# Kernel tuning notes

Hardware: AMD Instinct MI355X
Metric: run time of the kernel (lower is better)

Reference implementation:

```python
import jax, jax.numpy as jnp
import numpy as np

N_NODES = 50000
IN_DIM = 256
HID = 128
OUT_DIM = 64
N_LAYERS = 3
N_EDGES = 800000
BATCH = 4096
BN_EPS = 1e-5
LRELU_SLOPE = 0.01


def setup_inputs() -> dict:
    key = jax.random.key(0)
    ks = jax.random.split(key, 24)
    inp = {}
    inp["x"] = jax.random.normal(ks[0], (N_NODES, IN_DIM), jnp.float32)
    inp["edge_index"] = jax.random.randint(ks[1], (2, N_EDGES), 0, N_NODES, dtype=jnp.int32)
    inp["drug_pos_ids"] = jax.random.randint(ks[2], (BATCH,), 0, N_NODES, dtype=jnp.int32)
    inp["target_pos_ids"] = jax.random.randint(ks[3], (BATCH,), 0, N_NODES, dtype=jnp.int32)
    inp["drug_neg_ids"] = jax.random.randint(ks[4], (BATCH,), 0, N_NODES, dtype=jnp.int32)
    inp["target_neg_ids"] = jax.random.randint(ks[5], (BATCH,), 0, N_NODES, dtype=jnp.int32)
    inp["adjacency_matrix"] = jnp.zeros((1, 1), jnp.float32)  # dead arg in original forward
    # GCN layer params (xavier-normal-ish scale, zero bias as in __init__)
    for i in range(N_LAYERS):
        din = IN_DIM if i == 0 else HID
        inp[f"gcn_w{i}"] = jax.random.normal(ks[6 + i], (HID, din), jnp.float32) * np.float32(np.sqrt(2.0 / (din + HID)))
        inp[f"gcn_b{i}"] = jnp.zeros((HID,), jnp.float32)
    inp["bn_gamma"] = jnp.ones((HID,), jnp.float32)
    inp["bn_beta"] = jnp.zeros((HID,), jnp.float32)
    inp["W_D"] = jax.random.normal(ks[10], (HID, HID), jnp.float32) * np.float32(np.sqrt(2.0 / HID))
    inp["W_T"] = jax.random.normal(ks[11], (HID, HID), jnp.float32) * np.float32(np.sqrt(2.0 / HID))
    inp["q_D"] = jax.random.normal(ks[12], (HID,), jnp.float32)
    inp["q_T"] = jax.random.normal(ks[13], (HID,), jnp.float32)
    inp["out_w"] = jax.random.normal(ks[14], (OUT_DIM, HID), jnp.float32) * np.float32(np.sqrt(1.0 / HID))
    inp["out_b"] = jnp.zeros((OUT_DIM,), jnp.float32)
    return inp


def gcn_conv(x, w, b, src, dst, num_nodes):
    # PyG GCNConv: h = x @ W^T, then symmetric-normalized aggregation with self-loops
    h = x @ w.T                                           # [N, HID]
    deg = 1.0 + jax.ops.segment_sum(jnp.ones(src.shape[0], h.dtype), dst, num_segments=num_nodes)
    dinv = jax.lax.rsqrt(deg)                             # [N]
    norm = dinv[src] * dinv[dst]                          # [E]
    agg = jax.ops.segment_sum(h[src] * norm[:, None], dst, num_segments=num_nodes)
    agg = agg + h * (dinv * dinv)[:, None]                # self-loop contribution
    return agg + b


def batchnorm(x, gamma, beta):
    # training-mode BatchNorm1d math (batch statistics, biased var)
    mean = jnp.mean(x, axis=0)
    var = jnp.mean(jnp.square(x - mean), axis=0)
    return (x - mean) * jax.lax.rsqrt(var + BN_EPS) * gamma + beta


def attention_pooling(emb, W, q):
    # emb: [L, N, H]; softmax over the layer axis L
    h = jax.nn.leaky_relu(jnp.einsum('lnh,kh->lnk', emb, W), negative_slope=LRELU_SLOPE)
    e = jnp.einsum('lnk,k->ln', h, q)                     # [L, N]
    alpha = jax.nn.softmax(e, axis=0)
    return jnp.einsum('lnh,ln->nh', emb, alpha)           # [N, H]


def reference(x, edge_index, drug_pos_ids, target_pos_ids, drug_neg_ids, target_neg_ids,
              adjacency_matrix, gcn_w0, gcn_b0, gcn_w1, gcn_b1, gcn_w2, gcn_b2,
              bn_gamma, bn_beta, W_D, W_T, q_D, q_T, out_w, out_b):
    src, dst = edge_index[0], edge_index[1]
    num_nodes = x.shape[0]
    gcn_params = [(gcn_w0, gcn_b0), (gcn_w1, gcn_b1), (gcn_w2, gcn_b2)]
    layer_embs = []
    h = x
    for w, b in gcn_params:
        h = jax.nn.relu(gcn_conv(h, w, b, src, dst, num_nodes))
        h = batchnorm(h, bn_gamma, bn_beta)
        # dropout: identity (eval mode)
        layer_embs.append(h)
    emb = jnp.stack(layer_embs, axis=0)                   # [L, N, H]
    z_D = attention_pooling(emb, W_D, q_D) @ out_w.T + out_b
    z_T = attention_pooling(emb, W_T, q_T) @ out_w.T + out_b
    return (z_D[drug_pos_ids], z_T[target_pos_ids], z_D[drug_neg_ids], z_T[target_neg_ids])
```

## Files before the change

kernel.cpp:

```cpp
#include <hip/hip_runtime.h>
#include <hip/hip_fp16.h>
#include <cstdint>

#define N_NODES 50000
#define IN_DIM  256
#define HID     128
#define OUT_DIM 64
#define N_EDGES 800000
#define BATCH   4096
#define BN_EPS  1e-5f
#define SLOPE   0.01f

typedef unsigned short u16;
typedef __attribute__((ext_vector_type(8))) short bf16x8;
typedef __attribute__((ext_vector_type(4))) float f32x4;

__device__ __forceinline__ u16 f2bf(float f) {
    union { float f; unsigned u; } v; v.f = f;
    unsigned r = v.u + 0x7FFF + ((v.u >> 16) & 1);
    return (u16)(r >> 16);
}
__device__ __forceinline__ float bf2f(u16 b) {
    union { unsigned u; float f; } v; v.u = ((unsigned)b) << 16;
    return v.f;
}
__device__ __forceinline__ void splitbf(float v, u16* hi, u16* lo) {
    u16 h = f2bf(v);
    *hi = h;
    *lo = f2bf(v - bf2f(h));
}

__device__ __forceinline__ void swz_store(u16* __restrict__ buf, int K, int n, int k, float v) {
    int KC = K >> 7;
    int chunk = (n >> 6) * KC + (k >> 7);
    int base = chunk * 16384 + ((n >> 4) & 3) * 2048 + ((k >> 5) & 3) * 512
             + (((k >> 3) & 3) * 16 + (n & 15)) * 8 + (k & 7);
    u16 hi, lo;
    splitbf(v, &hi, &lo);
    buf[base] = hi;
    buf[base + 8192] = lo;
}

#define BNP_SPREAD 64
#define BNACC_PER_LAYER (BNP_SPREAD * 256)


#define PW0 (HID * IN_DIM)
#define PW1 (PW0 + HID * HID)
#define PW2 (PW1 + HID * HID)
#define PWD (PW2 + HID * HID)
#define PWT (PWD + HID * HID)
#define POW (PWT + OUT_DIM * HID)
#define PBN (POW + 3 * BNACC_PER_LAYER)
#define PBC (PBN + 256)
#define PTOT (PBC + 2 * 3 * 2 * BATCH)

__global__ void prep(const float* __restrict__ w0, const float* __restrict__ w1,
                     const float* __restrict__ w2, const float* __restrict__ WD,
                     const float* __restrict__ WT, const float* __restrict__ out_w,
                     u16* __restrict__ w0swz, u16* __restrict__ w1swz, u16* __restrict__ w2swz,
                     u16* __restrict__ wDTswz,
                     float* __restrict__ wt, float* __restrict__ bnacc3,
                     int* __restrict__ bucketCnt, float* __restrict__ ebuf) {
    int i = blockIdx.x * 256 + threadIdx.x;
    if (i < PW0) {
        swz_store(w0swz, IN_DIM, i >> 8, i & 255, w0[i]);
    } else if (i < PW1) {
        int j = i - PW0; swz_store(w1swz, HID, j >> 7, j & 127, w1[j]);
    } else if (i < PW2) {
        int j = i - PW1; swz_store(w2swz, HID, j >> 7, j & 127, w2[j]);
    } else if (i < PWD) {
        int j = i - PW2; swz_store(wDTswz, HID, j >> 7, j & 127, WD[j]);
    } else if (i < PWT) {
        int j = i - PWD; swz_store(wDTswz + 32768, HID, j >> 7, j & 127, WT[j]);
    } else if (i < POW) {
        int j = i - PWT;
        wt[j] = out_w[(j & 63) * HID + (j >> 6)];
    } else if (i < PBN) {
        bnacc3[i - POW] = 0.f;
    } else if (i < PBC) {
        bucketCnt[i - PBN] = 0;
    } else if (i < PTOT) {
        ebuf[i - PBC] = 0.f;
    }
}


#define NBKT 196
#define PASSA_CHUNK 2048
#define NB_A ((N_EDGES + PASSA_CHUNK - 1) / PASSA_CHUNK)

__global__ void bucket_count(const int* __restrict__ dst, int* __restrict__ bucketCnt) {
    __shared__ int hist[NBKT];
    int t = threadIdx.x;
    if (t < NBKT) hist[t] = 0;
    __syncthreads();
    int b0 = blockIdx.x * PASSA_CHUNK;
    int b1 = min(b0 + PASSA_CHUNK, N_EDGES);
    for (int i = b0 + t; i < b1; i += 256)
        atomicAdd(&hist[dst[i] >> 8], 1);
    __syncthreads();
    if (t < NBKT && hist[t] > 0) atomicAdd(&bucketCnt[t], hist[t]);
}

__global__ void bucket_scan(const int* __restrict__ bucketCnt, int* __restrict__ bucketBase,
                            int* __restrict__ gcursor, int* __restrict__ rowstart) {
    __shared__ int s[256];
    int t = threadIdx.x;
    int v = (t < NBKT) ? bucketCnt[t] : 0;
    s[t] = v;
    __syncthreads();
#pragma unroll
    for (int off = 1; off < 256; off <<= 1) {
        int tmp = (t >= off) ? s[t - off] : 0;
        __syncthreads();
        s[t] += tmp;
        __syncthreads();
    }
    if (t < NBKT) { bucketBase[t] = s[t] - v; gcursor[t] = s[t] - v; }
    if (t == 0) { bucketBase[NBKT] = N_EDGES; rowstart[N_NODES] = N_EDGES; }
}

__global__ void bucket_scatter(const int* __restrict__ src, const int* __restrict__ dst,
                               int* __restrict__ gcursor, unsigned* __restrict__ pairs) {
    __shared__ int hist[NBKT], base[NBKT], hist2[NBKT];
    int t = threadIdx.x;
    if (t < NBKT) { hist[t] = 0; hist2[t] = 0; }
    __syncthreads();
    int b0 = blockIdx.x * PASSA_CHUNK;
    int b1 = min(b0 + PASSA_CHUNK, N_EDGES);
    for (int i = b0 + t; i < b1; i += 256)
        atomicAdd(&hist[dst[i] >> 8], 1);
    __syncthreads();
    if (t < NBKT && hist[t] > 0) base[t] = atomicAdd(&gcursor[t], hist[t]);
    __syncthreads();
    for (int i = b0 + t; i < b1; i += 256) {
        int d = dst[i];
        int b = d >> 8;
        int lp = atomicAdd(&hist2[b], 1);
        pairs[base[b] + lp] = ((unsigned)(d & 255) << 16) | (unsigned)src[i];
    }
}

__global__ void bucket_build(const unsigned* __restrict__ pairs, const int* __restrict__ bucketBase,
                             int* __restrict__ rowstart, float* __restrict__ dinv,
                             u16* __restrict__ csr) {
    __shared__ int cnt[256], s[256], lcur[256];
    int b = blockIdx.x, t = threadIdx.x;
    int pb0 = bucketBase[b], pb1 = bucketBase[b + 1];
    cnt[t] = 0;
    __syncthreads();
    for (int i = pb0 + t; i < pb1; i += 256)
        atomicAdd(&cnt[pairs[i] >> 16], 1);
    __syncthreads();
    int v = cnt[t];
    s[t] = v;
    __syncthreads();
#pragma unroll
    for (int off = 1; off < 256; off <<= 1) {
        int tmp = (t >= off) ? s[t - off] : 0;
        __syncthreads();
        s[t] += tmp;
        __syncthreads();
    }
    int node = (b << 8) + t;
    int start = pb0 + s[t] - v;
    if (node < N_NODES) {
        rowstart[node] = start;
        dinv[node] = rsqrtf(1.0f + (float)v);
    }
    lcur[t] = start;
    __syncthreads();
    for (int i = pb0 + t; i < pb1; i += 256) {
        unsigned pr = pairs[i];
        int pos = atomicAdd(&lcur[pr >> 16], 1);
        csr[pos] = (u16)(pr & 0xFFFFu);
    }
}


__global__ __launch_bounds__(256) void gemm_tile(const float* __restrict__ A,
                                                 const float* __restrict__ bnss,
                                                 const u16* __restrict__ Bswz,
                                                 const float* __restrict__ dinv,
                                                 u16* __restrict__ Cout,
                                                 int M, int K) {
    __shared__ u16 Bs[32768];
    const int tid  = threadIdx.x;
    const int wave = tid >> 6, lane = tid & 63;
    const int lr   = lane & 15, quad = lane >> 4;
    const int rowBase = blockIdx.x * 64;
    const int KC = K >> 7;

    f32x4 acc[8];
#pragma unroll
    for (int c = 0; c < 8; ++c) acc[c] = (f32x4){0.f, 0.f, 0.f, 0.f};

    const int arow = rowBase + wave * 16 + lr;
    const bool rv = arow < M;

    for (int kc = 0; kc < KC; ++kc) {
        if (kc) __syncthreads();
        const uint4* s0 = (const uint4*)(Bswz + (size_t)kc * 16384);
        const uint4* s1 = (const uint4*)(Bswz + (size_t)(KC + kc) * 16384);
        uint4* B4 = (uint4*)Bs;
#pragma unroll
        for (int i = 0; i < 8; ++i)
            B4[i * 256 + tid] = s0[i * 256 + tid];
#pragma unroll
        for (int i = 0; i < 8; ++i)
            B4[2048 + i * 256 + tid] = s1[i * 256 + tid];
        __syncthreads();

#pragma unroll
        for (int kkidx = 0; kkidx < 4; ++kkidx) {
            const int kcol = kc * 128 + kkidx * 32 + quad * 8;
            float av[8];
            if (rv) {
                const float* ap = A + (size_t)arow * K + kcol;
                float4 v0 = ((const float4*)ap)[0];
                float4 v1 = ((const float4*)ap)[1];
                av[0] = v0.x; av[1] = v0.y; av[2] = v0.z; av[3] = v0.w;
                av[4] = v1.x; av[5] = v1.y; av[6] = v1.z; av[7] = v1.w;
            } else {
#pragma unroll
                for (int j = 0; j < 8; ++j) av[j] = 0.f;
            }
            if (bnss) {
#pragma unroll
                for (int j = 0; j < 8; ++j) {
                    float sc = bnss[kcol + j];
                    float sh = bnss[K + kcol + j];
                    av[j] = fmaf(av[j], sc, sh);
                }
            }
            bf16x8 ah, al;
#pragma unroll
            for (int j = 0; j < 8; ++j) {
                u16 hi, lo;
                splitbf(av[j], &hi, &lo);
                ((u16*)&ah)[j] = hi; ((u16*)&al)[j] = lo;
            }
#pragma unroll
            for (int c = 0; c < 8; ++c) {
                const int lb = (c >> 2) * 16384 + (c & 3) * 2048 + kkidx * 512 + lane * 8;
                bf16x8 bh = *(const bf16x8*)&Bs[lb];
                bf16x8 bl = *(const bf16x8*)&Bs[lb + 8192];
                acc[c] = __builtin_amdgcn_mfma_f32_16x16x32_bf16(al, bh, acc[c], 0, 0, 0);
                acc[c] = __builtin_amdgcn_mfma_f32_16x16x32_bf16(ah, bl, acc[c], 0, 0, 0);
                acc[c] = __builtin_amdgcn_mfma_f32_16x16x32_bf16(ah, bh, acc[c], 0, 0, 0);
            }
        }
    }

    const int rowb = rowBase + wave * 16 + quad * 4;
#pragma unroll
    for (int reg = 0; reg < 4; ++reg) {
        int row = rowb + reg;
        if (row < M) {
            float dn = dinv[row];
#pragma unroll
            for (int c = 0; c < 8; ++c) {
                __half hv = __float2half(acc[c][reg] * dn);
                Cout[(size_t)row * 128 + c * 16 + lr] = *(u16*)&hv;
            }
        }
    }
}


__global__ __launch_bounds__(256) void pool_gemm(const float* __restrict__ emb0,
                                                 const float* __restrict__ emb1,
                                                 const float* __restrict__ emb2,
                                                 const float* __restrict__ bnss3,
                                                 const int* __restrict__ dpos, const int* __restrict__ dneg,
                                                 const int* __restrict__ tpos, const int* __restrict__ tneg,
                                                 const u16* __restrict__ wDTswz,
                                                 const float* __restrict__ q_D, const float* __restrict__ q_T,
                                                 float* __restrict__ e_D, float* __restrict__ e_T) {
    __shared__ u16 Bs[32768];
    const int head = blockIdx.y;
    const u16* Bswz = wDTswz + head * 32768;
    const float* q  = head ? q_T : q_D;
    float* eo = head ? e_T : e_D;
    const int* ia = head ? tpos : dpos;
    const int* ib = head ? tneg : dneg;

    const int tid  = threadIdx.x;
    const int wave = tid >> 6, lane = tid & 63;
    const int lr   = lane & 15, quad = lane >> 4;
    const int rowBase = blockIdx.x * 64;

    const int arow = rowBase + wave * 16 + lr;
    const int l0 = arow >> 13, j0 = arow & 8191;
    const int node0 = (j0 < BATCH) ? ia[j0] : ib[j0 - BATCH];
    const float* embs[3] = {emb0, emb1, emb2};
    const float* A0 = embs[l0] + (size_t)node0 * HID;
    const float* bn0 = bnss3 + l0 * 2 * HID;

    f32x4 acc[8];
#pragma unroll
    for (int c = 0; c < 8; ++c) acc[c] = (f32x4){0.f, 0.f, 0.f, 0.f};

    uint4* B4 = (uint4*)Bs;
    const uint4* srcB = (const uint4*)Bswz;
#pragma unroll
    for (int i = 0; i < 16; ++i)
        B4[i * 256 + tid] = srcB[i * 256 + tid];
    __syncthreads();

#pragma unroll
    for (int kkidx = 0; kkidx < 4; ++kkidx) {
        const int kcol = kkidx * 32 + quad * 8;
        float av[8];
        {
            float4 v0 = ((const float4*)(A0 + kcol))[0];
            float4 v1 = ((const float4*)(A0 + kcol))[1];
            av[0] = v0.x; av[1] = v0.y; av[2] = v0.z; av[3] = v0.w;
            av[4] = v1.x; av[5] = v1.y; av[6] = v1.z; av[7] = v1.w;
        }
#pragma unroll
        for (int j = 0; j < 8; ++j)
            av[j] = fmaf(av[j], bn0[kcol + j], bn0[HID + kcol + j]);
        bf16x8 ah, al;
#pragma unroll
        for (int j = 0; j < 8; ++j) {
            u16 hi, lo;
            splitbf(av[j], &hi, &lo);
            ((u16*)&ah)[j] = hi; ((u16*)&al)[j] = lo;
        }
#pragma unroll
        for (int c = 0; c < 8; ++c) {
            const int lb = (c >> 2) * 16384 + (c & 3) * 2048 + kkidx * 512 + lane * 8;
            bf16x8 bh = *(const bf16x8*)&Bs[lb];
            bf16x8 bl = *(const bf16x8*)&Bs[lb + 8192];
            acc[c] = __builtin_amdgcn_mfma_f32_16x16x32_bf16(al, bh, acc[c], 0, 0, 0);
            acc[c] = __builtin_amdgcn_mfma_f32_16x16x32_bf16(ah, bl, acc[c], 0, 0, 0);
            acc[c] = __builtin_amdgcn_mfma_f32_16x16x32_bf16(ah, bh, acc[c], 0, 0, 0);
        }
    }

    float qv[8];
#pragma unroll
    for (int c = 0; c < 8; ++c) qv[c] = q[c * 16 + lr];
    const int rowb = rowBase + wave * 16 + quad * 4;
#pragma unroll
    for (int reg = 0; reg < 4; ++reg) {
        float p = 0.f;
#pragma unroll
        for (int c = 0; c < 8; ++c) {
            float v = acc[c][reg];
            v = (v > 0.f) ? v : SLOPE * v;
            p = fmaf(v, qv[c], p);
        }
        p += __shfl_xor(p, 1);
        p += __shfl_xor(p, 2);
        p += __shfl_xor(p, 4);
        p += __shfl_xor(p, 8);
        if (lr == 0) eo[rowb + reg] = p;
    }
}


__global__ __launch_bounds__(256) void agg_relu(const u16* __restrict__ h,
                                                const float* __restrict__ dinv,
                                                const int* __restrict__ rowstart,
                                                const u16* __restrict__ csr,
                                                const float* __restrict__ bias,
                                                float* __restrict__ out,
                                                float* __restrict__ bnpart) {
    __shared__ float s_s[HID], s_sq[HID];
    int tid  = threadIdx.x;
    int wave = tid >> 6;
    int lane = tid & 63;
    int slot = lane >> 4;
    int q    = lane & 15;
    if (tid < HID) { s_s[tid] = 0.f; s_sq[tid] = 0.f; }
    __syncthreads();

    float bs[8], bq[8];
#pragma unroll
    for (int j = 0; j < 8; ++j) { bs[j] = 0.f; bq[j] = 0.f; }

    int n = blockIdx.x * 16 + wave * 4 + slot;
    if (n < N_NODES) {
        int s = rowstart[n], e1 = rowstart[n + 1];
        float a[8];
#pragma unroll
        for (int j = 0; j < 8; ++j) a[j] = 0.f;

        int e = s;
        for (; e + 3 < e1; e += 4) {
            int c0 = csr[e], c1 = csr[e + 1], c2 = csr[e + 2], c3 = csr[e + 3];
            uint4 w0 = ((const uint4*)(h + (size_t)c0 * HID))[q];
            uint4 w1 = ((const uint4*)(h + (size_t)c1 * HID))[q];
            uint4 w2 = ((const uint4*)(h + (size_t)c2 * HID))[q];
            uint4 w3 = ((const uint4*)(h + (size_t)c3 * HID))[q];
            {
                float2 p0 = __half22float2(*(const __half2*)&w0.x);
                float2 p1 = __half22float2(*(const __half2*)&w0.y);
                float2 p2 = __half22float2(*(const __half2*)&w0.z);
                float2 p3 = __half22float2(*(const __half2*)&w0.w);
                a[0] += p0.x; a[1] += p0.y; a[2] += p1.x; a[3] += p1.y;
                a[4] += p2.x; a[5] += p2.y; a[6] += p3.x; a[7] += p3.y;
            }
            {
                float2 p0 = __half22float2(*(const __half2*)&w1.x);
                float2 p1 = __half22float2(*(const __half2*)&w1.y);
                float2 p2 = __half22float2(*(const __half2*)&w1.z);
                float2 p3 = __half22float2(*(const __half2*)&w1.w);
                a[0] += p0.x; a[1] += p0.y; a[2] += p1.x; a[3] += p1.y;
                a[4] += p2.x; a[5] += p2.y; a[6] += p3.x; a[7] += p3.y;
            }
            {
                float2 p0 = __half22float2(*(const __half2*)&w2.x);
                float2 p1 = __half22float2(*(const __half2*)&w2.y);
                float2 p2 = __half22float2(*(const __half2*)&w2.z);
                float2 p3 = __half22float2(*(const __half2*)&w2.w);
                a[0] += p0.x; a[1] += p0.y; a[2] += p1.x; a[3] += p1.y;
                a[4] += p2.x; a[5] += p2.y; a[6] += p3.x; a[7] += p3.y;
            }
            {
                float2 p0 = __half22float2(*(const __half2*)&w3.x);
                float2 p1 = __half22float2(*(const __half2*)&w3.y);
                float2 p2 = __half22float2(*(const __half2*)&w3.z);
                float2 p3 = __half22float2(*(const __half2*)&w3.w);
                a[0] += p0.x; a[1] += p0.y; a[2] += p1.x; a[3] += p1.y;
                a[4] += p2.x; a[5] += p2.y; a[6] += p3.x; a[7] += p3.y;
            }
        }
        for (; e < e1; ++e) {
            int c0 = csr[e];
            uint4 w0 = ((const uint4*)(h + (size_t)c0 * HID))[q];
            float2 p0 = __half22float2(*(const __half2*)&w0.x);
            float2 p1 = __half22float2(*(const __half2*)&w0.y);
            float2 p2 = __half22float2(*(const __half2*)&w0.z);
            float2 p3 = __half22float2(*(const __half2*)&w0.w);
            a[0] += p0.x; a[1] += p0.y; a[2] += p1.x; a[3] += p1.y;
            a[4] += p2.x; a[5] += p2.y; a[6] += p3.x; a[7] += p3.y;
        }

        float dn = dinv[n];
        uint4 hw = ((const uint4*)(h + (size_t)n * HID))[q];
        float2 h0 = __half22float2(*(const __half2*)&hw.x);
        float2 h1 = __half22float2(*(const __half2*)&hw.y);
        float2 h2 = __half22float2(*(const __half2*)&hw.z);
        float2 h3 = __half22float2(*(const __half2*)&hw.w);
        float hv[8] = {h0.x, h0.y, h1.x, h1.y, h2.x, h2.y, h3.x, h3.y};
        float4 bv0 = ((const float4*)bias)[2 * q];
        float4 bv1 = ((const float4*)bias)[2 * q + 1];
        float bb[8] = {bv0.x, bv0.y, bv0.z, bv0.w, bv1.x, bv1.y, bv1.z, bv1.w};
        float o[8];
#pragma unroll
        for (int j = 0; j < 8; ++j) {
            o[j] = fmaxf(fmaf(dn, a[j] + hv[j], bb[j]), 0.f);
            bs[j] += o[j];
            bq[j] = fmaf(o[j], o[j], bq[j]);
        }
        float4 o0 = {o[0], o[1], o[2], o[3]};
        float4 o1 = {o[4], o[5], o[6], o[7]};
        ((float4*)(out + (size_t)n * HID))[2 * q]     = o0;
        ((float4*)(out + (size_t)n * HID))[2 * q + 1] = o1;
    }

#pragma unroll
    for (int j = 0; j < 8; ++j) {
        bs[j] += __shfl_xor(bs[j], 16);
        bs[j] += __shfl_xor(bs[j], 32);
        bq[j] += __shfl_xor(bq[j], 16);
        bq[j] += __shfl_xor(bq[j], 32);
    }
    if (slot == 0) {
#pragma unroll
        for (int j = 0; j < 8; ++j) {
            atomicAdd(&s_s[q * 8 + j], bs[j]);
            atomicAdd(&s_sq[q * 8 + j], bq[j]);
        }
    }
    __syncthreads();
    float* bp = bnpart + (size_t)(blockIdx.x & (BNP_SPREAD - 1)) * 256;
    if (tid < HID) atomicAdd(&bp[tid], s_s[tid]);
    else           atomicAdd(&bp[tid], s_sq[tid - HID]);
}

__global__ void bn_finalize(const float* __restrict__ acc,
                            const float* __restrict__ gamma, const float* __restrict__ beta,
                            float* __restrict__ bnss) {
    int f = threadIdx.x;
    float st = 0.f, sqt = 0.f;
    for (int p = 0; p < BNP_SPREAD; ++p) {
        st  += acc[p * 256 + f];
        sqt += acc[p * 256 + HID + f];
    }
    float mean = st * (1.0f / N_NODES);
    float var  = fmaxf(sqt * (1.0f / N_NODES) - mean * mean, 0.f);
    float sc   = gamma[f] * rsqrtf(var + BN_EPS);
    bnss[f] = sc;
    bnss[HID + f] = beta[f] - mean * sc;
}


__global__ void softmax_pool(const float* __restrict__ e0, const float* __restrict__ e1,
                             const float* __restrict__ e2, const float* __restrict__ bnss3,
                             const int* __restrict__ dpos, const int* __restrict__ dneg,
                             const int* __restrict__ tpos, const int* __restrict__ tneg,
                             const float* __restrict__ e_D, const float* __restrict__ e_T,
                             float* __restrict__ P_D, float* __restrict__ P_T) {
    int j = blockIdx.x;
    int f = threadIdx.x;
    int head = blockIdx.y;
    const int* ia = head ? tpos : dpos;
    const int* ib = head ? tneg : dneg;
    const float* e = head ? e_T : e_D;
    float* P = head ? P_T : P_D;
    int node = (j < BATCH) ? ia[j] : ib[j - BATCH];
    float l0 = e[j], l1 = e[2 * BATCH + j], l2 = e[4 * BATCH + j];
    float m = fmaxf(l0, fmaxf(l1, l2));
    float a0 = expf(l0 - m), a1 = expf(l1 - m), a2 = expf(l2 - m);
    float inv = 1.0f / (a0 + a1 + a2);
    float v0 = fmaf(e0[(size_t)node * HID + f], bnss3[f],           bnss3[HID + f]);
    float v1 = fmaf(e1[(size_t)node * HID + f], bnss3[2 * HID + f], bnss3[3 * HID + f]);
    float v2 = fmaf(e2[(size_t)node * HID + f], bnss3[4 * HID + f], bnss3[5 * HID + f]);
    P[(size_t)j * HID + f] = (a0 * v0 + a1 * v1 + a2 * v2) * inv;
}


__global__ __launch_bounds__(256) void head_gemm(const float* __restrict__ P_D,
                                                 const float* __restrict__ P_T,
                                                 const float* __restrict__ B,
                                                 const float* __restrict__ bias,
                                                 float* __restrict__ out) {
    constexpr int BM = 64, BK = 32, BN = OUT_DIM, TM = 4, TN = 4;
    __shared__ float As[BK][BM];
    __shared__ float Bs[BK][BN];
    const int y = blockIdx.y;
    const float* A = ((y & 1) ? P_T : P_D) + (size_t)(y >> 1) * BATCH * HID;
    float* C = out + (size_t)y * BATCH * OUT_DIM;
    const int tid = threadIdx.x;
    const int tx = tid & 15, ty = tid >> 4;
    const int rowBase = blockIdx.x * BM;
    float acc[TM][TN];
#pragma unroll
    for (int i = 0; i < TM; ++i)
#pragma unroll
        for (int j = 0; j < TN; ++j) acc[i][j] = 0.f;

    for (int kk = 0; kk < HID; kk += BK) {
#pragma unroll
        for (int i = tid; i < (BM * BK) / 4; i += 256) {
            int m  = i >> 3;
            int kq = i & 7;
            float4 v = *(const float4*)(A + (size_t)(rowBase + m) * HID + kk + kq * 4);
            As[kq * 4 + 0][m] = v.x;
            As[kq * 4 + 1][m] = v.y;
            As[kq * 4 + 2][m] = v.z;
            As[kq * 4 + 3][m] = v.w;
        }
#pragma unroll
        for (int i = tid; i < (BK * BN) / 4; i += 256) {
            int k  = i / (BN / 4);
            int n4 = i % (BN / 4);
            *(float4*)&Bs[k][n4 * 4] = *(const float4*)(B + (size_t)(kk + k) * BN + n4 * 4);
        }
        __syncthreads();
#pragma unroll 8
        for (int k = 0; k < BK; ++k) {
            float a[TM], b[TN];
#pragma unroll
            for (int i = 0; i < TM; ++i) a[i] = As[k][ty * TM + i];
#pragma unroll
            for (int j = 0; j < TN; ++j) b[j] = Bs[k][tx * TN + j];
#pragma unroll
            for (int i = 0; i < TM; ++i)
#pragma unroll
                for (int j = 0; j < TN; ++j)
                    acc[i][j] = fmaf(a[i], b[j], acc[i][j]);
        }
        __syncthreads();
    }
#pragma unroll
    for (int i = 0; i < TM; ++i) {
        int grow = rowBase + ty * TM + i;
#pragma unroll
        for (int j = 0; j < TN; ++j)
            C[(size_t)grow * BN + tx * TN + j] = acc[i][j] + bias[tx * TN + j];
    }
}


extern "C" void kernel_launch(void* const* d_in, const int* in_sizes, int n_in,
                              void* d_out, int out_size, void* d_ws, size_t ws_size,
                              hipStream_t stream) {
    const float* x          = (const float*)d_in[0];
    const int*   ei         = (const int*)d_in[1];
    const int*   srcp       = ei;
    const int*   dstp       = ei + N_EDGES;
    const int*   drug_pos   = (const int*)d_in[2];
    const int*   target_pos = (const int*)d_in[3];
    const int*   drug_neg   = (const int*)d_in[4];
    const int*   target_neg = (const int*)d_in[5];
    const float* gcn_w[3]   = {(const float*)d_in[7], (const float*)d_in[9], (const float*)d_in[11]};
    const float* gcn_b[3]   = {(const float*)d_in[8], (const float*)d_in[10], (const float*)d_in[12]};
    const float* gamma      = (const float*)d_in[13];
    const float* beta       = (const float*)d_in[14];
    const float* W_D        = (const float*)d_in[15];
    const float* W_T        = (const float*)d_in[16];
    const float* q_D        = (const float*)d_in[17];
    const float* q_T        = (const float*)d_in[18];
    const float* out_w      = (const float*)d_in[19];
    const float* out_b      = (const float*)d_in[20];
    float*       out        = (float*)d_out;

    char* p = (char*)d_ws;
    auto alloc = [&](size_t bytes) -> char* {
        char* r = p;
        p += (bytes + 255) & ~(size_t)255;
        return r;
    };
    char*  reg1  = alloc(sizeof(float) * (size_t)N_NODES * HID);
    float* emb0  = (float*)alloc(sizeof(float) * (size_t)N_NODES * HID);
    float* emb1  = (float*)alloc(sizeof(float) * (size_t)N_NODES * HID);
    float* emb2  = (float*)alloc(sizeof(float) * (size_t)N_NODES * HID);
    float* ebuf  = (float*)alloc(sizeof(float) * (size_t)2 * 3 * 2 * BATCH);
    u16*   w0swz = (u16*)alloc(sizeof(u16) * 2 * HID * IN_DIM);
    u16*   w1swz = (u16*)alloc(sizeof(u16) * 2 * HID * HID);
    u16*   w2swz = (u16*)alloc(sizeof(u16) * 2 * HID * HID);
    u16*   wDTswz = (u16*)alloc(sizeof(u16) * 4 * HID * HID);
    float* wt    = (float*)alloc(sizeof(float) * OUT_DIM * HID);
    int*   rowstart = (int*)alloc(sizeof(int) * (N_NODES + 1));
    u16*   csr   = (u16*)alloc(sizeof(int) * N_EDGES);
    unsigned* pairs = (unsigned*)alloc(sizeof(unsigned) * N_EDGES);
    float* dinvp = (float*)alloc(sizeof(float) * N_NODES);
    int*   bucketCnt  = (int*)alloc(sizeof(int) * 256);
    int*   bucketBase = (int*)alloc(sizeof(int) * (NBKT + 1));
    int*   gcursor    = (int*)alloc(sizeof(int) * 256);
    float* bnacc3 = (float*)alloc(sizeof(float) * 3 * BNACC_PER_LAYER);
    float* bnss3  = (float*)alloc(sizeof(float) * 3 * 2 * HID);
    if ((size_t)(p - (char*)d_ws) > ws_size) return;

    u16*   hbuf = (u16*)reg1;
    float* P_D  = (float*)reg1;
    float* P_T  = P_D + (size_t)2 * BATCH * HID;
    float* e_D  = ebuf;
    float* e_T  = ebuf + 3 * 2 * BATCH;
    float* embp[3] = {emb0, emb1, emb2};
    const u16* wswz[3] = {w0swz, w1swz, w2swz};

    prep<<<(PTOT + 255) / 256, 256, 0, stream>>>(
        gcn_w[0], gcn_w[1], gcn_w[2], W_D, W_T, out_w,
        w0swz, w1swz, w2swz, wDTswz, wt, bnacc3, bucketCnt, ebuf);

    bucket_count<<<NB_A, 256, 0, stream>>>(dstp, bucketCnt);
    bucket_scan<<<1, 256, 0, stream>>>(bucketCnt, bucketBase, gcursor, rowstart);
    bucket_scatter<<<NB_A, 256, 0, stream>>>(srcp, dstp, gcursor, pairs);
    bucket_build<<<NBKT, 256, 0, stream>>>(pairs, bucketBase, rowstart, dinvp, csr);

    const int GB = (N_NODES + 63) / 64;
    for (int l = 0; l < 3; ++l) {
        int din = (l == 0) ? IN_DIM : HID;
        const float* Ain = (l == 0) ? x : embp[l - 1];
        const float* bnss = (l == 0) ? nullptr : (bnss3 + (l - 1) * 2 * HID);
        gemm_tile<<<GB, 256, 0, stream>>>(Ain, bnss, wswz[l], dinvp, hbuf, N_NODES, din);
        agg_relu<<<(N_NODES + 15) / 16, 256, 0, stream>>>(hbuf, dinvp, rowstart, csr, gcn_b[l],
                                                          embp[l], bnacc3 + l * BNACC_PER_LAYER);
        bn_finalize<<<1, HID, 0, stream>>>(bnacc3 + l * BNACC_PER_LAYER, gamma, beta,
                                           bnss3 + l * 2 * HID);
    }

    const int RG = 3 * 2 * BATCH;
    pool_gemm<<<dim3(RG / 64, 2), 256, 0, stream>>>(
        emb0, emb1, emb2, bnss3, drug_pos, drug_neg, target_pos, target_neg,
        wDTswz, q_D, q_T, e_D, e_T);
    softmax_pool<<<dim3(2 * BATCH, 2), HID, 0, stream>>>(
        emb0, emb1, emb2, bnss3, drug_pos, drug_neg, target_pos, target_neg,
        e_D, e_T, P_D, P_T);

    head_gemm<<<dim3(BATCH / 64, 4), 256, 0, stream>>>(P_D, P_T, wt, out_b, out);
}
```

Baseline: 397.9 us.

## Fuse softmax pooling into output head GEMM and use nontemporal embedding stores

Merges the softmax-weighted pooling of the three layer embeddings into the head GEMM kernel. Each block now builds its 64x128 pooled tile directly in shared memory instead of writing P_D/P_T to global memory and reading them back, which also removes one kernel launch. The block count for the head drops from 16384 small blocks to 256 larger ones, so gather parallelism is lower. Separately, agg_relu writes its embedding output with nontemporal stores, which risks cache misses when later kernels read those embeddings.

```diff
diff --git a/kernel.cpp b/kernel.cpp
--- a/kernel.cpp
+++ b/kernel.cpp
@@ -457,10 +457,10 @@
             bs[j] += o[j];
             bq[j] = fmaf(o[j], o[j], bq[j]);
         }
-        float4 o0 = {o[0], o[1], o[2], o[3]};
-        float4 o1 = {o[4], o[5], o[6], o[7]};
-        ((float4*)(out + (size_t)n * HID))[2 * q]     = o0;
-        ((float4*)(out + (size_t)n * HID))[2 * q + 1] = o1;
+        f32x4 o0 = {o[0], o[1], o[2], o[3]};
+        f32x4 o1 = {o[4], o[5], o[6], o[7]};
+        __builtin_nontemporal_store(o0, (f32x4*)(out + (size_t)n * HID) + 2 * q);
+        __builtin_nontemporal_store(o1, (f32x4*)(out + (size_t)n * HID) + 2 * q + 1);
     }
 
 #pragma unroll
@@ -500,90 +500,96 @@
 }
 
 
-__global__ void softmax_pool(const float* __restrict__ e0, const float* __restrict__ e1,
-                             const float* __restrict__ e2, const float* __restrict__ bnss3,
-                             const int* __restrict__ dpos, const int* __restrict__ dneg,
-                             const int* __restrict__ tpos, const int* __restrict__ tneg,
-                             const float* __restrict__ e_D, const float* __restrict__ e_T,
-                             float* __restrict__ P_D, float* __restrict__ P_T) {
-    int j = blockIdx.x;
-    int f = threadIdx.x;
-    int head = blockIdx.y;
+__global__ __launch_bounds__(256) void head_fused(const float* __restrict__ emb0,
+                                                  const float* __restrict__ emb1,
+                                                  const float* __restrict__ emb2,
+                                                  const float* __restrict__ bnss3,
+                                                  const int* __restrict__ dpos, const int* __restrict__ dneg,
+                                                  const int* __restrict__ tpos, const int* __restrict__ tneg,
+                                                  const float* __restrict__ e_D, const float* __restrict__ e_T,
+                                                  const float* __restrict__ B,
+                                                  const float* __restrict__ bias,
+                                                  float* __restrict__ out) {
+    __shared__ float Pl[HID][64];
+    __shared__ float Bs[32][OUT_DIM];
+    const int y = blockIdx.y;
+    const int head = y & 1, seg = y >> 1;
     const int* ia = head ? tpos : dpos;
     const int* ib = head ? tneg : dneg;
     const float* e = head ? e_T : e_D;
-    float* P = head ? P_T : P_D;
-    int node = (j < BATCH) ? ia[j] : ib[j - BATCH];
-    float l0 = e[j], l1 = e[2 * BATCH + j], l2 = e[4 * BATCH + j];
-    float m = fmaxf(l0, fmaxf(l1, l2));
-    float a0 = expf(l0 - m), a1 = expf(l1 - m), a2 = expf(l2 - m);
-    float inv = 1.0f / (a0 + a1 + a2);
-    float v0 = fmaf(e0[(size_t)node * HID + f], bnss3[f],           bnss3[HID + f]);
-    float v1 = fmaf(e1[(size_t)node * HID + f], bnss3[2 * HID + f], bnss3[3 * HID + f]);
-    float v2 = fmaf(e2[(size_t)node * HID + f], bnss3[4 * HID + f], bnss3[5 * HID + f]);
-    P[(size_t)j * HID + f] = (a0 * v0 + a1 * v1 + a2 * v2) * inv;
-}
-
-
-__global__ __launch_bounds__(256) void head_gemm(const float* __restrict__ P_D,
-                                                 const float* __restrict__ P_T,
-                                                 const float* __restrict__ B,
-                                                 const float* __restrict__ bias,
-                                                 float* __restrict__ out) {
-    constexpr int BM = 64, BK = 32, BN = OUT_DIM, TM = 4, TN = 4;
-    __shared__ float As[BK][BM];
-    __shared__ float Bs[BK][BN];
-    const int y = blockIdx.y;
-    const float* A = ((y & 1) ? P_T : P_D) + (size_t)(y >> 1) * BATCH * HID;
-    float* C = out + (size_t)y * BATCH * OUT_DIM;
     const int tid = threadIdx.x;
+
+    {
+        int r = tid >> 2;
+        int part = tid & 3;
+        int p = seg * BATCH + blockIdx.x * 64 + r;
+        int node = (p < BATCH) ? ia[p] : ib[p - BATCH];
+        float l0 = e[p], l1 = e[2 * BATCH + p], l2 = e[4 * BATCH + p];
+        float m = fmaxf(l0, fmaxf(l1, l2));
+        float a0 = expf(l0 - m), a1 = expf(l1 - m), a2 = expf(l2 - m);
+        float inv = 1.0f / (a0 + a1 + a2);
+        a0 *= inv; a1 *= inv; a2 *= inv;
+        const float* r0 = emb0 + (size_t)node * HID + part * 32;
+        const float* r1 = emb1 + (size_t)node * HID + part * 32;
+        const float* r2 = emb2 + (size_t)node * HID + part * 32;
+#pragma unroll
+        for (int c = 0; c < 32; c += 4) {
+            float4 v0 = *(const float4*)(r0 + c);
+            float4 v1 = *(const float4*)(r1 + c);
+            float4 v2 = *(const float4*)(r2 + c);
+            int f = part * 32 + c;
+            float e0v[4] = {v0.x, v0.y, v0.z, v0.w};
+            float e1v[4] = {v1.x, v1.y, v1.z, v1.w};
+            float e2v[4] = {v2.x, v2.y, v2.z, v2.w};
+#pragma unroll
+            for (int u = 0; u < 4; ++u) {
+                float b0 = fmaf(e0v[u], bnss3[f + u],           bnss3[HID + f + u]);
+                float b1 = fmaf(e1v[u], bnss3[2 * HID + f + u], bnss3[3 * HID + f + u]);
+                float b2 = fmaf(e2v[u], bnss3[4 * HID + f + u], bnss3[5 * HID + f + u]);
+                Pl[f + u][r] = a0 * b0 + a1 * b1 + a2 * b2;
+            }
+        }
+    }
+    __syncthreads();
+
     const int tx = tid & 15, ty = tid >> 4;
-    const int rowBase = blockIdx.x * BM;
-    float acc[TM][TN];
-#pragma unroll
-    for (int i = 0; i < TM; ++i)
-#pragma unroll
-        for (int j = 0; j < TN; ++j) acc[i][j] = 0.f;
-
-    for (int kk = 0; kk < HID; kk += BK) {
-#pragma unroll
-        for (int i = tid; i < (BM * BK) / 4; i += 256) {
-            int m  = i >> 3;
-            int kq = i & 7;
-            float4 v = *(const float4*)(A + (size_t)(rowBase + m) * HID + kk + kq * 4);
-            As[kq * 4 + 0][m] = v.x;
-            As[kq * 4 + 1][m] = v.y;
-            As[kq * 4 + 2][m] = v.z;
-            As[kq * 4 + 3][m] = v.w;
-        }
-#pragma unroll
-        for (int i = tid; i < (BK * BN) / 4; i += 256) {
-            int k  = i / (BN / 4);
-            int n4 = i % (BN / 4);
-            *(float4*)&Bs[k][n4 * 4] = *(const float4*)(B + (size_t)(kk + k) * BN + n4 * 4);
+    float acc[4][4];
+#pragma unroll
+    for (int i = 0; i < 4; ++i)
+#pragma unroll
+        for (int j = 0; j < 4; ++j) acc[i][j] = 0.f;
+
+    for (int kk = 0; kk < HID; kk += 32) {
+        if (kk) __syncthreads();
+#pragma unroll
+        for (int i = tid; i < (32 * OUT_DIM) / 4; i += 256) {
+            int k  = i >> 4;
+            int n4 = i & 15;
+            *(float4*)&Bs[k][n4 * 4] = *(const float4*)(B + (size_t)(kk + k) * OUT_DIM + n4 * 4);
         }
         __syncthreads();
 #pragma unroll 8
-        for (int k = 0; k < BK; ++k) {
-            float a[TM], b[TN];
-#pragma unroll
-            for (int i = 0; i < TM; ++i) a[i] = As[k][ty * TM + i];
-#pragma unroll
-            for (int j = 0; j < TN; ++j) b[j] = Bs[k][tx * TN + j];
-#pragma unroll
-            for (int i = 0; i < TM; ++i)
-#pragma unroll
-                for (int j = 0; j < TN; ++j)
+        for (int k = 0; k < 32; ++k) {
+            float a[4], b[4];
+#pragma unroll
+            for (int i = 0; i < 4; ++i) a[i] = Pl[kk + k][ty * 4 + i];
+#pragma unroll
+            for (int j = 0; j < 4; ++j) b[j] = Bs[k][tx * 4 + j];
+#pragma unroll
+            for (int i = 0; i < 4; ++i)
+#pragma unroll
+                for (int j = 0; j < 4; ++j)
                     acc[i][j] = fmaf(a[i], b[j], acc[i][j]);
         }
-        __syncthreads();
-    }
-#pragma unroll
-    for (int i = 0; i < TM; ++i) {
-        int grow = rowBase + ty * TM + i;
-#pragma unroll
-        for (int j = 0; j < TN; ++j)
-            C[(size_t)grow * BN + tx * TN + j] = acc[i][j] + bias[tx * TN + j];
+    }
+
+    float* C = out + (size_t)y * BATCH * OUT_DIM + (size_t)(blockIdx.x * 64) * OUT_DIM;
+#pragma unroll
+    for (int i = 0; i < 4; ++i) {
+        int r = ty * 4 + i;
+#pragma unroll
+        for (int j = 0; j < 4; ++j)
+            C[(size_t)r * OUT_DIM + tx * 4 + j] = acc[i][j] + bias[tx * 4 + j];
     }
 }
 
@@ -639,8 +645,6 @@
     if ((size_t)(p - (char*)d_ws) > ws_size) return;
 
     u16*   hbuf = (u16*)reg1;
-    float* P_D  = (float*)reg1;
-    float* P_T  = P_D + (size_t)2 * BATCH * HID;
     float* e_D  = ebuf;
     float* e_T  = ebuf + 3 * 2 * BATCH;
     float* embp[3] = {emb0, emb1, emb2};
@@ -671,9 +675,8 @@
     pool_gemm<<<dim3(RG / 64, 2), 256, 0, stream>>>(
         emb0, emb1, emb2, bnss3, drug_pos, drug_neg, target_pos, target_neg,
         wDTswz, q_D, q_T, e_D, e_T);
-    softmax_pool<<<dim3(2 * BATCH, 2), HID, 0, stream>>>(
+
+    head_fused<<<dim3(BATCH / 64, 4), 256, 0, stream>>>(
         emb0, emb1, emb2, bnss3, drug_pos, drug_neg, target_pos, target_neg,
-        e_D, e_T, P_D, P_T);
-
-    head_gemm<<<dim3(BATCH / 64, 4), 256, 0, stream>>>(P_D, P_T, wt, out_b, out);
-}
+        e_D, e_T, wt, out_b, out);
+}
```

Measured after the change: 397.5 us. Within noise of the previous version (-0.1%).
